# Kernel optimization log

Hardware: AMD Instinct MI355X
Metric: run time of the kernel (lower is better)

Reference implementation:

```python
import jax, jax.numpy as jnp
import numpy as np

B = 131072
IN_DIM = 21   # velocity_dim * (past_frame + 2) = 3 * 7
HID = 512
OUT_DIM = 21  # 7 waypoints * 3 coords
SEG = 0.5     # segment width in in_same_segment
WW = 0.5      # rescale weight for same-segment elements
INVALID = -10000.0
VALID_THRESH = -5000.0


def setup_inputs() -> dict:
    key = jax.random.key(0)
    ks = jax.random.split(key, 9)
    velocities = jax.random.normal(ks[0], (B, IN_DIM), dtype=jnp.float32)
    gt = jax.random.normal(ks[1], (B, 7, 3), dtype=jnp.float32)
    # emulate warp_gt padding: some trailing waypoints are invalid sentinels
    pad_mask = jax.random.bernoulli(ks[2], 0.2, (B, 7, 1))
    gt = jnp.where(pad_mask, jnp.float32(INVALID), gt)
    s1 = 1.0 / np.sqrt(IN_DIM)
    s2 = 1.0 / np.sqrt(HID)
    W1 = jax.random.uniform(ks[3], (HID, IN_DIM), jnp.float32, -s1, s1)
    b1 = jax.random.uniform(ks[4], (HID,), jnp.float32, -s1, s1)
    W2 = jax.random.uniform(ks[5], (HID, HID), jnp.float32, -s2, s2)
    b2 = jax.random.uniform(ks[6], (HID,), jnp.float32, -s2, s2)
    W3 = jax.random.uniform(ks[7], (OUT_DIM, HID), jnp.float32, -s2, s2)
    b3 = jax.random.uniform(ks[8], (OUT_DIM,), jnp.float32, -s2, s2)
    return {"velocities": velocities, "gt": gt,
            "W1": W1, "b1": b1, "W2": W2, "b2": b2, "W3": W3, "b3": b3}


def reference(velocities, gt, W1, b1, W2, b2, W3, b3):
    # plan_head MLP: 21 -> 512 -> 512 -> 21
    h = jax.nn.relu(velocities @ W1.T + b1)
    h = jax.nn.relu(h @ W2.T + b2)
    out = h @ W3.T + b3                      # [B, 21]
    pred = out.reshape(-1, 7, 3)             # waypoints x1..x7, 3 coords each
    # segment-conditional weighted L1 loss (vectorized form of the Python loop)
    valid = gt > VALID_THRESH
    same_seg = jnp.floor(pred / SEG) == jnp.floor(gt / SEG)
    w = jnp.where(valid & same_seg, jnp.float32(WW), jnp.float32(1.0))
    diff = jnp.abs(pred * w - gt * w)
    num = jnp.sum(jnp.where(valid, diff, 0.0))
    den = jnp.sum(valid.astype(jnp.float32))
    return num / den
```

## Files before the change

### kernel.cpp

```cpp
#include <hip/hip_runtime.h>
#include <hip/hip_bf16.h>

typedef __bf16 bf16_t;
typedef __bf16 bf16x4 __attribute__((ext_vector_type(4)));
typedef __bf16 bf16x8 __attribute__((ext_vector_type(8)));
typedef float f32x4 __attribute__((ext_vector_type(4)));

#define IN_DIM 21
#define HID 512
#define OUT_DIM 21
#define M_TILE 64
#define THREADS 512

__device__ __forceinline__ int swz(int row, int col) {
    return col ^ ((row & 7) << 3);
}

__global__ void prep_kernel(const float* __restrict__ W1, const float* __restrict__ W2,
                            const float* __restrict__ W3,
                            bf16_t* __restrict__ W1f, bf16_t* __restrict__ W2f,
                            bf16_t* __restrict__ W3f, float* __restrict__ accum) {
    if (blockIdx.x == 0 && threadIdx.x == 0) { accum[0] = 0.0f; accum[1] = 0.0f; }
    int i = blockIdx.x * blockDim.x + threadIdx.x;
    int stride = gridDim.x * blockDim.x;
    const int NW2 = HID * HID;
    const int NW1 = 32 * 512;
    const int NW3 = 16 * 2 * 512;
    for (; i < NW2 + NW1 + NW3; i += stride) {
        if (i < NW2) {
            int j = i & 7, lane = (i >> 3) & 63, ntile = (i >> 9) & 31, kstep = i >> 14;
            int n = ntile * 16 + (lane & 15);
            int k = kstep * 32 + (lane >> 4) * 8 + j;
            W2f[i] = (bf16_t)W2[n * HID + k];
        } else if (i < NW2 + NW1) {
            int t = i - NW2;
            int j = t & 7, lane = (t >> 3) & 63, ntile = t >> 9;
            int n = ntile * 16 + (lane & 15);
            int k = (lane >> 4) * 8 + j;
            W1f[t] = (k < IN_DIM) ? (bf16_t)W1[n * IN_DIM + k] : (bf16_t)0.0f;
        } else {
            int t = i - NW2 - NW1;
            int j = t & 7, lane = (t >> 3) & 63, ot = (t >> 9) & 1, kstep = t >> 10;
            int o = ot * 16 + (lane & 15);
            int k = kstep * 32 + (lane >> 4) * 8 + j;
            W3f[t] = (o < OUT_DIM) ? (bf16_t)W3[o * HID + k] : (bf16_t)0.0f;
        }
    }
}

__global__ __launch_bounds__(THREADS, 4)
void fused_kernel(const float* __restrict__ V, const float* __restrict__ gt,
                  const float* __restrict__ b1, const float* __restrict__ b2,
                  const float* __restrict__ b3,
                  const bf16_t* __restrict__ W1f, const bf16_t* __restrict__ W2f,
                  const bf16_t* __restrict__ W3f, float* __restrict__ accum) {
    __shared__ __align__(16) bf16_t vlds[M_TILE][40];
    __shared__ __align__(16) bf16_t h[M_TILE][HID];
    __shared__ float redbuf[16];

    const int tid  = threadIdx.x;
    const int wave = tid >> 6;
    const int lane = tid & 63;
    const int quad = lane >> 4;
    const int l16  = lane & 15;
    const int sx   = (l16 & 7) << 3;
    const long row0 = (long)blockIdx.x * M_TILE;

    for (int idx = tid; idx < M_TILE * 32; idx += THREADS) {
        int r = idx >> 5, c = idx & 31;
        float v = (c < IN_DIM) ? V[(row0 + r) * IN_DIM + c] : 0.0f;
        vlds[r][c] = (bf16_t)v;
    }
    __syncthreads();

    {
        bf16x8 bv[4];
        #pragma unroll
        for (int mt = 0; mt < 4; ++mt)
            bv[mt] = *reinterpret_cast<const bf16x8*>(&vlds[mt * 16 + l16][quad * 8]);
        #pragma unroll
        for (int nt = 0; nt < 4; ++nt) {
            int ntile = wave * 4 + nt;
            bf16x8 aw = *reinterpret_cast<const bf16x8*>(W1f + ntile * 512 + lane * 8);
            f32x4 bias = *reinterpret_cast<const f32x4*>(b1 + ntile * 16 + quad * 4);
            int n0 = ntile * 16 + quad * 4;
            #pragma unroll
            for (int mt = 0; mt < 4; ++mt) {
                f32x4 c = {0.0f, 0.0f, 0.0f, 0.0f};
                c = __builtin_amdgcn_mfma_f32_16x16x32_bf16(aw, bv[mt], c, 0, 0, 0);
                bf16x4 pk;
                #pragma unroll
                for (int r = 0; r < 4; ++r) {
                    float v = c[r] + bias[r];
                    pk[r] = (bf16_t)(v > 0.0f ? v : 0.0f);
                }
                int m = mt * 16 + l16;
                *reinterpret_cast<bf16x4*>(&h[m][n0 ^ sx]) = pk;
            }
        }
    }
    __syncthreads();

    {
        f32x4 acc[4][4];
        #pragma unroll
        for (int mt = 0; mt < 4; ++mt)
            #pragma unroll
            for (int nt = 0; nt < 4; ++nt)
                acc[mt][nt] = (f32x4){0.0f, 0.0f, 0.0f, 0.0f};

        const bf16_t* w2p = W2f + (wave * 4) * 512 + lane * 8;

        #pragma unroll 1
        for (int ks = 0; ks < 16; ++ks) {
            const bf16_t* wk = w2p + ks * 16384;
            bf16x8 aw[4];
            #pragma unroll
            for (int nt = 0; nt < 4; ++nt)
                aw[nt] = *reinterpret_cast<const bf16x8*>(wk + nt * 512);
            bf16x8 bh[4];
            #pragma unroll
            for (int mt = 0; mt < 4; ++mt)
                bh[mt] = *reinterpret_cast<const bf16x8*>(
                    &h[mt * 16 + l16][(ks * 32 + quad * 8) ^ sx]);
            #pragma unroll
            for (int mt = 0; mt < 4; ++mt)
                #pragma unroll
                for (int nt = 0; nt < 4; ++nt)
                    acc[mt][nt] = __builtin_amdgcn_mfma_f32_16x16x32_bf16(aw[nt], bh[mt], acc[mt][nt], 0, 0, 0);
        }
        __syncthreads();

        #pragma unroll
        for (int nt = 0; nt < 4; ++nt) {
            int ntile = wave * 4 + nt;
            f32x4 bias = *reinterpret_cast<const f32x4*>(b2 + ntile * 16 + quad * 4);
            int n0 = ntile * 16 + quad * 4;
            #pragma unroll
            for (int mt = 0; mt < 4; ++mt) {
                bf16x4 pk;
                #pragma unroll
                for (int r = 0; r < 4; ++r) {
                    float v = acc[mt][nt][r] + bias[r];
                    pk[r] = (bf16_t)(v > 0.0f ? v : 0.0f);
                }
                int m = mt * 16 + l16;
                *reinterpret_cast<bf16x4*>(&h[m][n0 ^ sx]) = pk;
            }
        }
    }
    __syncthreads();

    {
        const int mt = wave >> 1;
        const int ot = wave & 1;
        const int o0 = ot * 16 + quad * 4;
        const long grow = row0 + mt * 16 + l16;

        float g[4], b3v[4];
        #pragma unroll
        for (int r = 0; r < 4; ++r) {
            bool v = (o0 + r) < OUT_DIM;
            g[r]   = v ? gt[grow * OUT_DIM + o0 + r] : -10000.0f;
            b3v[r] = v ? b3[o0 + r] : 0.0f;
        }

        f32x4 acc3a = {0.0f, 0.0f, 0.0f, 0.0f};
        f32x4 acc3b = {0.0f, 0.0f, 0.0f, 0.0f};
        const int rr = mt * 16 + l16;
        #pragma unroll
        for (int ks = 0; ks < 16; ks += 2) {
            bf16x8 bh0 = *reinterpret_cast<const bf16x8*>(&h[rr][(ks * 32 + quad * 8) ^ sx]);
            bf16x8 bh1 = *reinterpret_cast<const bf16x8*>(&h[rr][((ks + 1) * 32 + quad * 8) ^ sx]);
            bf16x8 aw0 = *reinterpret_cast<const bf16x8*>(W3f + (ks * 2 + ot) * 512 + lane * 8);
            bf16x8 aw1 = *reinterpret_cast<const bf16x8*>(W3f + ((ks + 1) * 2 + ot) * 512 + lane * 8);
            acc3a = __builtin_amdgcn_mfma_f32_16x16x32_bf16(aw0, bh0, acc3a, 0, 0, 0);
            acc3b = __builtin_amdgcn_mfma_f32_16x16x32_bf16(aw1, bh1, acc3b, 0, 0, 0);
        }

        float num = 0.0f, den = 0.0f;
        #pragma unroll
        for (int r = 0; r < 4; ++r) {
            if ((o0 + r) < OUT_DIM) {
                float pred = acc3a[r] + acc3b[r] + b3v[r];
                if (g[r] > -5000.0f) {
                    float w = (floorf(pred * 2.0f) == floorf(g[r] * 2.0f)) ? 0.5f : 1.0f;
                    num += fabsf(pred * w - g[r] * w);
                    den += 1.0f;
                }
            }
        }
        #pragma unroll
        for (int off = 32; off > 0; off >>= 1) {
            num += __shfl_down(num, off);
            den += __shfl_down(den, off);
        }
        if (lane == 0) { redbuf[wave * 2] = num; redbuf[wave * 2 + 1] = den; }
    }
    __syncthreads();
    if (tid == 0) {
        float n8 = 0.0f, d8 = 0.0f;
        #pragma unroll
        for (int w = 0; w < 8; ++w) { n8 += redbuf[w * 2]; d8 += redbuf[w * 2 + 1]; }
        atomicAdd(accum, n8);
        atomicAdd(accum + 1, d8);
    }
}

__global__ void finalize_kernel(const float* __restrict__ accum, float* __restrict__ out) {
    if (threadIdx.x == 0) out[0] = accum[0] / accum[1];
}

extern "C" void kernel_launch(void* const* d_in, const int* in_sizes, int n_in,
                              void* d_out, int out_size, void* d_ws, size_t ws_size,
                              hipStream_t stream) {
    const float* V  = (const float*)d_in[0];
    const float* gt = (const float*)d_in[1];
    const float* W1 = (const float*)d_in[2];
    const float* b1 = (const float*)d_in[3];
    const float* W2 = (const float*)d_in[4];
    const float* b2 = (const float*)d_in[5];
    const float* W3 = (const float*)d_in[6];
    const float* b3 = (const float*)d_in[7];
    float* out = (float*)d_out;

    char* ws = (char*)d_ws;
    float* accum = (float*)ws;
    bf16_t* W2f = (bf16_t*)(ws + 16);
    bf16_t* W1f = (bf16_t*)(ws + 16 + 512 * 512 * 2);
    bf16_t* W3f = (bf16_t*)(ws + 16 + 512 * 512 * 2 + 32 * 512 * 2);

    int Brows = in_sizes[0] / IN_DIM;
    int grid = Brows / M_TILE;

    prep_kernel<<<576, 512, 0, stream>>>(W1, W2, W3, W1f, W2f, W3f, accum);
    fused_kernel<<<grid, THREADS, 0, stream>>>(V, gt, b1, b2, b3, W1f, W2f, W3f, accum);
    finalize_kernel<<<1, 64, 0, stream>>>(accum, out);
}
```

Before: 194.6 us.

## Double the row tile, double-buffer W2 register loads, fuse finalize into last block

Raises the row tile to 128 and the block to 1024 threads. The 16 waves split into two M halves by eight N groups, and they share one LDS hidden buffer. The W2 fragment loads are software-pipelined with two register buffers so global loads overlap the MFMA work of the previous k-step. The separate finalize launch is replaced by a last-block-done atomic counter that writes the final ratio. The hidden buffer now needs 128KB of LDS per block, which caps residency, and the unchanged launch bound with 1024 threads may force tight register limits or spills.

```diff
diff --git a/kernel.cpp b/kernel.cpp
--- a/kernel.cpp
+++ b/kernel.cpp
@@ -9,8 +9,8 @@
 #define IN_DIM 21
 #define HID 512
 #define OUT_DIM 21
-#define M_TILE 64
-#define THREADS 512
+#define M_TILE 128
+#define THREADS 1024
 
 __device__ __forceinline__ int swz(int row, int col) {
     return col ^ ((row & 7) << 3);
@@ -20,7 +20,10 @@
                             const float* __restrict__ W3,
                             bf16_t* __restrict__ W1f, bf16_t* __restrict__ W2f,
                             bf16_t* __restrict__ W3f, float* __restrict__ accum) {
-    if (blockIdx.x == 0 && threadIdx.x == 0) { accum[0] = 0.0f; accum[1] = 0.0f; }
+    if (blockIdx.x == 0 && threadIdx.x == 0) {
+        accum[0] = 0.0f; accum[1] = 0.0f;
+        ((unsigned*)accum)[2] = 0u;
+    }
     int i = blockIdx.x * blockDim.x + threadIdx.x;
     int stride = gridDim.x * blockDim.x;
     const int NW2 = HID * HID;
@@ -53,18 +56,27 @@
                   const float* __restrict__ b1, const float* __restrict__ b2,
                   const float* __restrict__ b3,
                   const bf16_t* __restrict__ W1f, const bf16_t* __restrict__ W2f,
-                  const bf16_t* __restrict__ W3f, float* __restrict__ accum) {
+                  const bf16_t* __restrict__ W3f, float* __restrict__ accum,
+                  float* __restrict__ out) {
     __shared__ __align__(16) bf16_t vlds[M_TILE][40];
     __shared__ __align__(16) bf16_t h[M_TILE][HID];
-    __shared__ float redbuf[16];
+    __shared__ float redbuf[32];
 
     const int tid  = threadIdx.x;
     const int wave = tid >> 6;
     const int lane = tid & 63;
     const int quad = lane >> 4;
     const int l16  = lane & 15;
+    const int mh   = wave >> 3;
+    const int ng   = wave & 7;
     const int sx   = (l16 & 7) << 3;
     const long row0 = (long)blockIdx.x * M_TILE;
+
+    const bf16_t* w2p = W2f + ng * 4 * 512 + lane * 8;
+    bf16x8 awA[4], awB[4];
+    #pragma unroll
+    for (int nt = 0; nt < 4; ++nt)
+        awA[nt] = *reinterpret_cast<const bf16x8*>(w2p + nt * 512);
 
     for (int idx = tid; idx < M_TILE * 32; idx += THREADS) {
         int r = idx >> 5, c = idx & 31;
@@ -77,10 +89,10 @@
         bf16x8 bv[4];
         #pragma unroll
         for (int mt = 0; mt < 4; ++mt)
-            bv[mt] = *reinterpret_cast<const bf16x8*>(&vlds[mt * 16 + l16][quad * 8]);
+            bv[mt] = *reinterpret_cast<const bf16x8*>(&vlds[mh * 64 + mt * 16 + l16][quad * 8]);
         #pragma unroll
         for (int nt = 0; nt < 4; ++nt) {
-            int ntile = wave * 4 + nt;
+            int ntile = ng * 4 + nt;
             bf16x8 aw = *reinterpret_cast<const bf16x8*>(W1f + ntile * 512 + lane * 8);
             f32x4 bias = *reinterpret_cast<const f32x4*>(b1 + ntile * 16 + quad * 4);
             int n0 = ntile * 16 + quad * 4;
@@ -94,7 +106,7 @@
                     float v = c[r] + bias[r];
                     pk[r] = (bf16_t)(v > 0.0f ? v : 0.0f);
                 }
-                int m = mt * 16 + l16;
+                int m = mh * 64 + mt * 16 + l16;
                 *reinterpret_cast<bf16x4*>(&h[m][n0 ^ sx]) = pk;
             }
         }
@@ -109,31 +121,44 @@
             for (int nt = 0; nt < 4; ++nt)
                 acc[mt][nt] = (f32x4){0.0f, 0.0f, 0.0f, 0.0f};
 
-        const bf16_t* w2p = W2f + (wave * 4) * 512 + lane * 8;
-
         #pragma unroll 1
-        for (int ks = 0; ks < 16; ++ks) {
-            const bf16_t* wk = w2p + ks * 16384;
-            bf16x8 aw[4];
+        for (int ks = 0; ks < 16; ks += 2) {
             #pragma unroll
             for (int nt = 0; nt < 4; ++nt)
-                aw[nt] = *reinterpret_cast<const bf16x8*>(wk + nt * 512);
-            bf16x8 bh[4];
-            #pragma unroll
-            for (int mt = 0; mt < 4; ++mt)
-                bh[mt] = *reinterpret_cast<const bf16x8*>(
-                    &h[mt * 16 + l16][(ks * 32 + quad * 8) ^ sx]);
-            #pragma unroll
-            for (int mt = 0; mt < 4; ++mt)
-                #pragma unroll
-                for (int nt = 0; nt < 4; ++nt)
-                    acc[mt][nt] = __builtin_amdgcn_mfma_f32_16x16x32_bf16(aw[nt], bh[mt], acc[mt][nt], 0, 0, 0);
+                awB[nt] = *reinterpret_cast<const bf16x8*>(w2p + (ks + 1) * 16384 + nt * 512);
+            {
+                bf16x8 bh[4];
+                #pragma unroll
+                for (int mt = 0; mt < 4; ++mt)
+                    bh[mt] = *reinterpret_cast<const bf16x8*>(
+                        &h[mh * 64 + mt * 16 + l16][(ks * 32 + quad * 8) ^ sx]);
+                #pragma unroll
+                for (int mt = 0; mt < 4; ++mt)
+                    #pragma unroll
+                    for (int nt = 0; nt < 4; ++nt)
+                        acc[mt][nt] = __builtin_amdgcn_mfma_f32_16x16x32_bf16(awA[nt], bh[mt], acc[mt][nt], 0, 0, 0);
+            }
+            #pragma unroll
+            for (int nt = 0; nt < 4; ++nt)
+                awA[nt] = *reinterpret_cast<const bf16x8*>(w2p + (ks + 2) * 16384 + nt * 512);
+            {
+                bf16x8 bh[4];
+                #pragma unroll
+                for (int mt = 0; mt < 4; ++mt)
+                    bh[mt] = *reinterpret_cast<const bf16x8*>(
+                        &h[mh * 64 + mt * 16 + l16][((ks + 1) * 32 + quad * 8) ^ sx]);
+                #pragma unroll
+                for (int mt = 0; mt < 4; ++mt)
+                    #pragma unroll
+                    for (int nt = 0; nt < 4; ++nt)
+                        acc[mt][nt] = __builtin_amdgcn_mfma_f32_16x16x32_bf16(awB[nt], bh[mt], acc[mt][nt], 0, 0, 0);
+            }
         }
         __syncthreads();
 
         #pragma unroll
         for (int nt = 0; nt < 4; ++nt) {
-            int ntile = wave * 4 + nt;
+            int ntile = ng * 4 + nt;
             f32x4 bias = *reinterpret_cast<const f32x4*>(b2 + ntile * 16 + quad * 4);
             int n0 = ntile * 16 + quad * 4;
             #pragma unroll
@@ -144,7 +169,7 @@
                     float v = acc[mt][nt][r] + bias[r];
                     pk[r] = (bf16_t)(v > 0.0f ? v : 0.0f);
                 }
-                int m = mt * 16 + l16;
+                int m = mh * 64 + mt * 16 + l16;
                 *reinterpret_cast<bf16x4*>(&h[m][n0 ^ sx]) = pk;
             }
         }
@@ -199,16 +224,20 @@
     }
     __syncthreads();
     if (tid == 0) {
-        float n8 = 0.0f, d8 = 0.0f;
-        #pragma unroll
-        for (int w = 0; w < 8; ++w) { n8 += redbuf[w * 2]; d8 += redbuf[w * 2 + 1]; }
-        atomicAdd(accum, n8);
-        atomicAdd(accum + 1, d8);
-    }
-}
-
-__global__ void finalize_kernel(const float* __restrict__ accum, float* __restrict__ out) {
-    if (threadIdx.x == 0) out[0] = accum[0] / accum[1];
+        float nB = 0.0f, dB = 0.0f;
+        #pragma unroll
+        for (int w = 0; w < 16; ++w) { nB += redbuf[w * 2]; dB += redbuf[w * 2 + 1]; }
+        atomicAdd(accum, nB);
+        atomicAdd(accum + 1, dB);
+        __threadfence();
+        unsigned prev = atomicAdd((unsigned*)(accum + 2), 1u);
+        if (prev == gridDim.x - 1) {
+            __threadfence();
+            float num = __hip_atomic_load(accum,     __ATOMIC_RELAXED, __HIP_MEMORY_SCOPE_AGENT);
+            float den = __hip_atomic_load(accum + 1, __ATOMIC_RELAXED, __HIP_MEMORY_SCOPE_AGENT);
+            out[0] = num / den;
+        }
+    }
 }
 
 extern "C" void kernel_launch(void* const* d_in, const int* in_sizes, int n_in,
@@ -234,6 +263,5 @@
     int grid = Brows / M_TILE;
 
     prep_kernel<<<576, 512, 0, stream>>>(W1, W2, W3, W1f, W2f, W3f, accum);
-    fused_kernel<<<grid, THREADS, 0, stream>>>(V, gt, b1, b2, b3, W1f, W2f, W3f, accum);
-    finalize_kernel<<<1, 64, 0, stream>>>(accum, out);
-}
+    fused_kernel<<<grid, THREADS, 0, stream>>>(V, gt, b1, b2, b3, W1f, W2f, W3f, accum, out);
+}
```

Measured after the change: 193.4 us. Within noise of the previous version (-0.6%).
